# Performance work log

Measured on AMD Instinct MI355X. Metric: run time of the kernel, lower is better.

Reference implementation:

```python
import jax, jax.numpy as jnp
import numpy as np


def _pairwise_sqdist(a, b):
    # a: [m, n, d], b: [m, n, d] -> M: [m, n, n], M[m,i,j] = ||a[m,i]-b[m,j]||^2
    # Use the expansion |a|^2 + |b|^2 - 2 a.b to avoid materializing the
    # [m, n, n, d] difference tensor; clamp tiny negatives from cancellation.
    a2 = jnp.sum(a * a, axis=-1)  # [m, n]
    b2 = jnp.sum(b * b, axis=-1)  # [m, n]
    ab = jnp.einsum('mid,mjd->mij', a, b)  # [m, n, n]
    return jnp.maximum(a2[:, :, None] + b2[:, None, :] - 2.0 * ab, 0.0)


def setup_inputs() -> dict:
    key = jax.random.key(0)
    k1, k2 = jax.random.split(key)
    template = jax.random.normal(k1, (16, 4096, 3), dtype=jnp.float32)
    source = jax.random.normal(k2, (16, 4096, 3), dtype=jnp.float32)
    return {"template": template, "source": source}


def reference(template, source):
    M = _pairwise_sqdist(template, source)  # [m, n, n]
    # min over template index (axis 1): nearest template point for each source point
    dist1 = jnp.mean(jnp.sqrt(jnp.min(M, axis=1)))
    # min over source index (axis 2): nearest source point for each template point
    dist2 = jnp.mean(jnp.sqrt(jnp.min(M, axis=2)))
    return (dist1 + dist2) / 2.0
```

## Files before the change

kernel.cpp:

```cpp
#include <hip/hip_runtime.h>

#define N_PTS   4096
#define N_BATCH 16
#define INV_CNT (1.0f / (2.0f * N_BATCH * N_PTS))
#define AROW_BYTES ((size_t)2 * N_BATCH * N_PTS * 16 * 2)
#define NBLK    1024

typedef _Float16 f16x8  __attribute__((ext_vector_type(8)));

__global__ __launch_bounds__(256) void prep_kernel(
    const float* __restrict__ tpl, const float* __restrict__ src,
    _Float16* __restrict__ arow, float* __restrict__ out) {
    int pt = blockIdx.x * 256 + threadIdx.x;
    if (pt == 0) out[0] = 0.0f;
    const float* p = (pt < 65536 ? tpl : src) + (size_t)(pt & 65535) * 3;
    float x = p[0], y = p[1], z = p[2];
    float o2 = fmaf(x, x, fmaf(y, y, z * z));
    _Float16 xh = (_Float16)x, yh = (_Float16)y, zh = (_Float16)z;
    _Float16 xl = (_Float16)(x - (float)xh);
    _Float16 yl = (_Float16)(y - (float)yh);
    _Float16 zl = (_Float16)(z - (float)zh);
    _Float16 o2h = (_Float16)o2;
    _Float16 o2l = (_Float16)(o2 - (float)o2h);
    const _Float16 m2 = (_Float16)-2.0f;
    f16x8 v0, v1;
    v0[0] = m2 * xh; v0[1] = m2 * yh; v0[2] = m2 * zh;
    v0[3] = m2 * xl; v0[4] = m2 * yl; v0[5] = m2 * zl;
    v0[6] = m2 * xh; v0[7] = m2 * yh;
    v1[0] = m2 * zh; v1[1] = o2h; v1[2] = o2l;
    v1[3] = (_Float16)0.0f; v1[4] = (_Float16)0.0f; v1[5] = (_Float16)0.0f;
    v1[6] = (_Float16)0.0f; v1[7] = (_Float16)0.0f;
    *(f16x8*)(arow + (size_t)pt * 16)     = v0;
    *(f16x8*)(arow + (size_t)pt * 16 + 8) = v1;
}

#define FD(a,x,y) "v_min3_f32 %[" #a "], v" #x ", v" #y ", %[" #a "]\n\t"
#define FOLD_D0 FD(acc0,32,33) FD(acc1,34,35) FD(acc0,36,37) FD(acc1,38,39) \
                FD(acc0,40,41) FD(acc1,42,43) FD(acc0,44,45) FD(acc1,46,47)
#define FOLD_D1 FD(acc0,48,49) FD(acc1,50,51) FD(acc0,52,53) FD(acc1,54,55) \
                FD(acc0,56,57) FD(acc1,58,59) FD(acc0,60,61) FD(acc1,62,63)
#define FOLD_D2 FD(acc0,64,65) FD(acc1,66,67) FD(acc0,68,69) FD(acc1,70,71) \
                FD(acc0,72,73) FD(acc1,74,75) FD(acc0,76,77) FD(acc1,78,79)
#define FOLD_D3 FD(acc0,80,81) FD(acc1,82,83) FD(acc0,84,85) FD(acc1,86,87) \
                FD(acc0,88,89) FD(acc1,90,91) FD(acc0,92,93) FD(acc1,94,95)
#define MF0(a) "v_mfma_f32_32x32x16_f16 v[32:47], %[" #a "], %[bf], v[96:111]\n\t"
#define MF1(a) "v_mfma_f32_32x32x16_f16 v[48:63], %[" #a "], %[bf], v[96:111]\n\t"
#define MF2(a) "v_mfma_f32_32x32x16_f16 v[64:79], %[" #a "], %[bf], v[96:111]\n\t"
#define MF3(a) "v_mfma_f32_32x32x16_f16 v[80:95], %[" #a "], %[bf], v[96:111]\n\t"
#define LD(a,off) "global_load_dwordx4 %[" #a "], %[voff], %[sb] offset:" #off "\n\t"
#define WNOP(n) "s_waitcnt vmcnt(" #n ")\n\t" "s_nop 1\n\t"
#define ZM(r) "v_mov_b32 v" #r ", 0\n\t"

__global__ __launch_bounds__(256, 4) void chamfer_mfma(
    const float* __restrict__ tpl, const float* __restrict__ src,
    const _Float16* __restrict__ arow, float* __restrict__ blocksum,
    float* __restrict__ out) {
    __shared__ float wsum[4];

    const int tid = threadIdx.x;
    const int wv = tid >> 6, lane = tid & 63;
    const int n = lane & 31, g = lane >> 5;
    const int qb = blockIdx.x, batch = blockIdx.y, dir = blockIdx.z;

    const float* qpts = (dir == 0) ? src : tpl;
    const _Float16* abase = arow + ((dir == 0) ? (size_t)0 : (size_t)65536 * 16)
                          + (size_t)batch * 4096 * 16;

    const int q = qb * 128 + wv * 32 + n;
    const float* p = qpts + (size_t)(batch * 4096 + q) * 3;
    float px = p[0], py = p[1], pz = p[2];
    float p2 = fmaf(px, px, fmaf(py, py, pz * pz));
    f16x8 bf;
    {
        _Float16 xh = (_Float16)px, yh = (_Float16)py, zh = (_Float16)pz;
        _Float16 xl = (_Float16)(px - (float)xh);
        _Float16 yl = (_Float16)(py - (float)yh);
        _Float16 zl = (_Float16)(pz - (float)zh);
        if (g == 0) {
            bf[0] = xh; bf[1] = yh; bf[2] = zh;
            bf[3] = xh; bf[4] = yh; bf[5] = zh;
            bf[6] = xl; bf[7] = yl;
        } else {
            bf[0] = zl; bf[1] = (_Float16)1.0f; bf[2] = (_Float16)1.0f;
            bf[3] = (_Float16)0.0f; bf[4] = (_Float16)0.0f; bf[5] = (_Float16)0.0f;
            bf[6] = (_Float16)0.0f; bf[7] = (_Float16)0.0f;
        }
    }

    int voff = n * 32 + g * 16;
    int cnt = 30;
    float acc0 = 1e30f, acc1 = 1e30f;
    f16x8 ra0, ra1, ra2, ra3;

    asm volatile(
        "s_waitcnt vmcnt(0)\n\t"
        ZM(96) ZM(97) ZM(98) ZM(99) ZM(100) ZM(101) ZM(102) ZM(103)
        ZM(104) ZM(105) ZM(106) ZM(107) ZM(108) ZM(109) ZM(110) ZM(111)
        LD(a0,0) LD(a1,1024) LD(a2,2048) LD(a3,3072)
        "v_add_u32 %[voff], 0x1000, %[voff]\n\t"
        "s_waitcnt vmcnt(3)\n\t" MF0(a0) LD(a0,0)
        "s_waitcnt vmcnt(3)\n\t" MF1(a1) LD(a1,1024)
        "s_waitcnt vmcnt(3)\n\t" MF2(a2) LD(a2,2048)
        "s_waitcnt vmcnt(3)\n\t" MF3(a3) LD(a3,3072)
        "L_cham_%=:\n\t"
        "v_add_u32 %[voff], 0x1000, %[voff]\n\t"
        FOLD_D0 WNOP(3) MF0(a0) LD(a0,0)
        FOLD_D1 WNOP(3) MF1(a1) LD(a1,1024)
        FOLD_D2 WNOP(3) MF2(a2) LD(a2,2048)
        FOLD_D3 WNOP(3) MF3(a3) LD(a3,3072)
        "s_sub_u32 %[cnt], %[cnt], 1\n\t"
        "s_cmp_lg_u32 %[cnt], 0\n\t"
        "s_cbranch_scc1 L_cham_%=\n\t"
        FOLD_D0 WNOP(3) MF0(a0)
        FOLD_D1 WNOP(2) MF1(a1)
        FOLD_D2 WNOP(1) MF2(a2)
        FOLD_D3 WNOP(0) MF3(a3)
        FOLD_D0 FOLD_D1 FOLD_D2 FOLD_D3
        : [a0]"=&v"(ra0), [a1]"=&v"(ra1), [a2]"=&v"(ra2), [a3]"=&v"(ra3),
          [voff]"+v"(voff), [cnt]"+s"(cnt), [acc0]"+v"(acc0), [acc1]"+v"(acc1)
        : [bf]"v"(bf), [sb]"s"(abase)
        : "memory", "scc",
          "v32","v33","v34","v35","v36","v37","v38","v39",
          "v40","v41","v42","v43","v44","v45","v46","v47",
          "v48","v49","v50","v51","v52","v53","v54","v55",
          "v56","v57","v58","v59","v60","v61","v62","v63",
          "v64","v65","v66","v67","v68","v69","v70","v71",
          "v72","v73","v74","v75","v76","v77","v78","v79",
          "v80","v81","v82","v83","v84","v85","v86","v87",
          "v88","v89","v90","v91","v92","v93","v94","v95",
          "v96","v97","v98","v99","v100","v101","v102","v103",
          "v104","v105","v106","v107","v108","v109","v110","v111");

    float v = fminf(acc0, acc1);
    v = fminf(v, __shfl_xor(v, 32));
    float d = fmaxf(v + p2, 0.0f);
    float s = sqrtf(d) * INV_CNT;
    if (g != 0) s = 0.0f;
    #pragma unroll
    for (int off = 32; off > 0; off >>= 1) s += __shfl_down(s, off);
    if (lane == 0) wsum[wv] = s;
    __syncthreads();
    if (tid == 0) {
        float t = wsum[0] + wsum[1] + wsum[2] + wsum[3];
        if (blocksum) {
            int flat = (blockIdx.z * N_BATCH + blockIdx.y) * 32 + blockIdx.x;
            blocksum[flat] = t;
        } else {
            atomicAdd(out, t);
        }
    }
}

__global__ __launch_bounds__(256) void final_kernel(
    const float* __restrict__ blocksum, float* __restrict__ out) {
    __shared__ float wsum[4];
    float s = 0.0f;
    #pragma unroll
    for (int j = 0; j < NBLK / 256; ++j)
        s += blocksum[j * 256 + threadIdx.x];
    #pragma unroll
    for (int off = 32; off > 0; off >>= 1) s += __shfl_down(s, off);
    if ((threadIdx.x & 63) == 0) wsum[threadIdx.x >> 6] = s;
    __syncthreads();
    if (threadIdx.x == 0) out[0] = wsum[0] + wsum[1] + wsum[2] + wsum[3];
}

extern "C" void kernel_launch(void* const* d_in, const int* in_sizes, int n_in,
                              void* d_out, int out_size, void* d_ws, size_t ws_size,
                              hipStream_t stream) {
    const float* tpl = (const float*)d_in[0];
    const float* src = (const float*)d_in[1];
    float* out = (float*)d_out;
    _Float16* arow = (_Float16*)d_ws;
    const bool roomy = ws_size >= AROW_BYTES + NBLK * sizeof(float);
    float* blocksum = roomy ? (float*)((char*)d_ws + AROW_BYTES) : nullptr;

    hipLaunchKernelGGL(prep_kernel, dim3((2 * N_BATCH * N_PTS) / 256),
                       dim3(256), 0, stream, tpl, src, arow, out);
    dim3 grid(N_PTS / 128, N_BATCH, 2);
    hipLaunchKernelGGL(chamfer_mfma, grid, dim3(256), 0, stream,
                       tpl, src, arow, blocksum, out);
    if (roomy)
        hipLaunchKernelGGL(final_kernel, dim3(1), dim3(256), 0, stream,
                           blocksum, out);
}
```

Measured before the change: 81.22 us.

## Process two query tiles per wave to reuse loaded A rows across MFMAs

Each wave now handles 64 query points (two B fragments), so every loaded 32-row A tile feeds two MFMAs, halving global loads per MFMA. The pipeline is restructured to eight in-flight loads with interleaved min-folds of the previous tile's accumulators, and the grid is halved, with NBLK and the blocksum indexing updated to match. Occupancy is lowered to 2 waves-per-SIMD bound, and the prefetch overruns the row buffer, so blocksum is moved 8 KB further into the workspace.

```diff
diff --git a/kernel.cpp b/kernel.cpp
--- a/kernel.cpp
+++ b/kernel.cpp
@@ -4,7 +4,7 @@
 #define N_BATCH 16
 #define INV_CNT (1.0f / (2.0f * N_BATCH * N_PTS))
 #define AROW_BYTES ((size_t)2 * N_BATCH * N_PTS * 16 * 2)
-#define NBLK    1024
+#define NBLK    512
 
 typedef _Float16 f16x8  __attribute__((ext_vector_type(8)));
 
@@ -35,23 +35,27 @@
 }
 
 #define FD(a,x,y) "v_min3_f32 %[" #a "], v" #x ", v" #y ", %[" #a "]\n\t"
-#define FOLD_D0 FD(acc0,32,33) FD(acc1,34,35) FD(acc0,36,37) FD(acc1,38,39) \
-                FD(acc0,40,41) FD(acc1,42,43) FD(acc0,44,45) FD(acc1,46,47)
-#define FOLD_D1 FD(acc0,48,49) FD(acc1,50,51) FD(acc0,52,53) FD(acc1,54,55) \
-                FD(acc0,56,57) FD(acc1,58,59) FD(acc0,60,61) FD(acc1,62,63)
-#define FOLD_D2 FD(acc0,64,65) FD(acc1,66,67) FD(acc0,68,69) FD(acc1,70,71) \
-                FD(acc0,72,73) FD(acc1,74,75) FD(acc0,76,77) FD(acc1,78,79)
-#define FOLD_D3 FD(acc0,80,81) FD(acc1,82,83) FD(acc0,84,85) FD(acc1,86,87) \
-                FD(acc0,88,89) FD(acc1,90,91) FD(acc0,92,93) FD(acc1,94,95)
-#define MF0(a) "v_mfma_f32_32x32x16_f16 v[32:47], %[" #a "], %[bf], v[96:111]\n\t"
-#define MF1(a) "v_mfma_f32_32x32x16_f16 v[48:63], %[" #a "], %[bf], v[96:111]\n\t"
-#define MF2(a) "v_mfma_f32_32x32x16_f16 v[64:79], %[" #a "], %[bf], v[96:111]\n\t"
-#define MF3(a) "v_mfma_f32_32x32x16_f16 v[80:95], %[" #a "], %[bf], v[96:111]\n\t"
-#define LD(a,off) "global_load_dwordx4 %[" #a "], %[voff], %[sb] offset:" #off "\n\t"
-#define WNOP(n) "s_waitcnt vmcnt(" #n ")\n\t" "s_nop 1\n\t"
-#define ZM(r) "v_mov_b32 v" #r ", 0\n\t"
+#define FOLD_D0A FD(acc0,32,33) FD(acc1,34,35) FD(acc0,36,37) FD(acc1,38,39) \
+                 FD(acc0,40,41) FD(acc1,42,43) FD(acc0,44,45) FD(acc1,46,47)
+#define FOLD_D0B FD(acc0,48,49) FD(acc1,50,51) FD(acc0,52,53) FD(acc1,54,55) \
+                 FD(acc0,56,57) FD(acc1,58,59) FD(acc0,60,61) FD(acc1,62,63)
+#define FOLD_D1A FD(acc2,64,65) FD(acc3,66,67) FD(acc2,68,69) FD(acc3,70,71) \
+                 FD(acc2,72,73) FD(acc3,74,75) FD(acc2,76,77) FD(acc3,78,79)
+#define FOLD_D1B FD(acc2,80,81) FD(acc3,82,83) FD(acc2,84,85) FD(acc3,86,87) \
+                 FD(acc2,88,89) FD(acc3,90,91) FD(acc2,92,93) FD(acc3,94,95)
+#define LD(s,off) "global_load_dwordx4 %[" #s "], %[voff], %[sb] offset:" #off "\n\t"
+#define TILE_E(s,off) "s_waitcnt vmcnt(7)\n\t" \
+  "v_mfma_f32_32x32x16_f16 v[32:47], %[" #s "], %[bf0], v[96:111]\n\t" \
+  "v_mfma_f32_32x32x16_f16 v[64:79], %[" #s "], %[bf1], v[96:111]\n\t" \
+  LD(s,off) FOLD_D0B FOLD_D1B
+#define TILE_O(s,off) "s_waitcnt vmcnt(7)\n\t" \
+  "v_mfma_f32_32x32x16_f16 v[48:63], %[" #s "], %[bf0], v[96:111]\n\t" \
+  "v_mfma_f32_32x32x16_f16 v[80:95], %[" #s "], %[bf1], v[96:111]\n\t" \
+  LD(s,off) FOLD_D0A FOLD_D1A
+#define ZM(r)  "v_mov_b32 v" #r ", 0\n\t"
+#define IM(r)  "v_mov_b32 v" #r ", 0x7f800000\n\t"
 
-__global__ __launch_bounds__(256, 4) void chamfer_mfma(
+__global__ __launch_bounds__(256, 2) void chamfer_mfma(
     const float* __restrict__ tpl, const float* __restrict__ src,
     const _Float16* __restrict__ arow, float* __restrict__ blocksum,
     float* __restrict__ out) {
@@ -66,59 +70,63 @@
     const _Float16* abase = arow + ((dir == 0) ? (size_t)0 : (size_t)65536 * 16)
                           + (size_t)batch * 4096 * 16;
 
-    const int q = qb * 128 + wv * 32 + n;
-    const float* p = qpts + (size_t)(batch * 4096 + q) * 3;
-    float px = p[0], py = p[1], pz = p[2];
-    float p2 = fmaf(px, px, fmaf(py, py, pz * pz));
-    f16x8 bf;
-    {
+    f16x8 bfr[2];
+    float p2[2];
+    #pragma unroll
+    for (int i = 0; i < 2; ++i) {
+        const int q = qb * 256 + wv * 64 + i * 32 + n;
+        const float* p = qpts + (size_t)(batch * 4096 + q) * 3;
+        float px = p[0], py = p[1], pz = p[2];
+        p2[i] = fmaf(px, px, fmaf(py, py, pz * pz));
         _Float16 xh = (_Float16)px, yh = (_Float16)py, zh = (_Float16)pz;
         _Float16 xl = (_Float16)(px - (float)xh);
         _Float16 yl = (_Float16)(py - (float)yh);
         _Float16 zl = (_Float16)(pz - (float)zh);
+        f16x8 b;
         if (g == 0) {
-            bf[0] = xh; bf[1] = yh; bf[2] = zh;
-            bf[3] = xh; bf[4] = yh; bf[5] = zh;
-            bf[6] = xl; bf[7] = yl;
+            b[0] = xh; b[1] = yh; b[2] = zh;
+            b[3] = xh; b[4] = yh; b[5] = zh;
+            b[6] = xl; b[7] = yl;
         } else {
-            bf[0] = zl; bf[1] = (_Float16)1.0f; bf[2] = (_Float16)1.0f;
-            bf[3] = (_Float16)0.0f; bf[4] = (_Float16)0.0f; bf[5] = (_Float16)0.0f;
-            bf[6] = (_Float16)0.0f; bf[7] = (_Float16)0.0f;
+            b[0] = zl; b[1] = (_Float16)1.0f; b[2] = (_Float16)1.0f;
+            b[3] = (_Float16)0.0f; b[4] = (_Float16)0.0f; b[5] = (_Float16)0.0f;
+            b[6] = (_Float16)0.0f; b[7] = (_Float16)0.0f;
         }
+        bfr[i] = b;
     }
 
     int voff = n * 32 + g * 16;
-    int cnt = 30;
-    float acc0 = 1e30f, acc1 = 1e30f;
-    f16x8 ra0, ra1, ra2, ra3;
+    int cnt = 16;
+    float acc0 = 1e30f, acc1 = 1e30f, acc2 = 1e30f, acc3 = 1e30f;
+    f16x8 r0, r1, r2, r3, r4, r5, r6, r7;
 
     asm volatile(
-        "s_waitcnt vmcnt(0)\n\t"
         ZM(96) ZM(97) ZM(98) ZM(99) ZM(100) ZM(101) ZM(102) ZM(103)
         ZM(104) ZM(105) ZM(106) ZM(107) ZM(108) ZM(109) ZM(110) ZM(111)
-        LD(a0,0) LD(a1,1024) LD(a2,2048) LD(a3,3072)
+        IM(48) IM(49) IM(50) IM(51) IM(52) IM(53) IM(54) IM(55)
+        IM(56) IM(57) IM(58) IM(59) IM(60) IM(61) IM(62) IM(63)
+        IM(80) IM(81) IM(82) IM(83) IM(84) IM(85) IM(86) IM(87)
+        IM(88) IM(89) IM(90) IM(91) IM(92) IM(93) IM(94) IM(95)
+        LD(r0,0) LD(r1,1024) LD(r2,2048) LD(r3,3072)
         "v_add_u32 %[voff], 0x1000, %[voff]\n\t"
-        "s_waitcnt vmcnt(3)\n\t" MF0(a0) LD(a0,0)
-        "s_waitcnt vmcnt(3)\n\t" MF1(a1) LD(a1,1024)
-        "s_waitcnt vmcnt(3)\n\t" MF2(a2) LD(a2,2048)
-        "s_waitcnt vmcnt(3)\n\t" MF3(a3) LD(a3,3072)
+        LD(r4,0) LD(r5,1024) LD(r6,2048) LD(r7,3072)
+        "v_add_u32 %[voff], 0x1000, %[voff]\n\t"
         "L_cham_%=:\n\t"
+        TILE_E(r0,0) TILE_O(r1,1024) TILE_E(r2,2048) TILE_O(r3,3072)
         "v_add_u32 %[voff], 0x1000, %[voff]\n\t"
-        FOLD_D0 WNOP(3) MF0(a0) LD(a0,0)
-        FOLD_D1 WNOP(3) MF1(a1) LD(a1,1024)
-        FOLD_D2 WNOP(3) MF2(a2) LD(a2,2048)
-        FOLD_D3 WNOP(3) MF3(a3) LD(a3,3072)
+        TILE_E(r4,0) TILE_O(r5,1024) TILE_E(r6,2048) TILE_O(r7,3072)
+        "v_add_u32 %[voff], 0x1000, %[voff]\n\t"
         "s_sub_u32 %[cnt], %[cnt], 1\n\t"
         "s_cmp_lg_u32 %[cnt], 0\n\t"
         "s_cbranch_scc1 L_cham_%=\n\t"
-        FOLD_D0 WNOP(3) MF0(a0)
-        FOLD_D1 WNOP(2) MF1(a1)
-        FOLD_D2 WNOP(1) MF2(a2)
-        FOLD_D3 WNOP(0) MF3(a3)
-        FOLD_D0 FOLD_D1 FOLD_D2 FOLD_D3
-        : [a0]"=&v"(ra0), [a1]"=&v"(ra1), [a2]"=&v"(ra2), [a3]"=&v"(ra3),
-          [voff]"+v"(voff), [cnt]"+s"(cnt), [acc0]"+v"(acc0), [acc1]"+v"(acc1)
-        : [bf]"v"(bf), [sb]"s"(abase)
+        "s_nop 7\n\t" "s_nop 7\n\t" "s_nop 7\n\t"
+        FOLD_D0B FOLD_D1B
+        "s_waitcnt vmcnt(0)\n\t"
+        : [r0]"=&v"(r0), [r1]"=&v"(r1), [r2]"=&v"(r2), [r3]"=&v"(r3),
+          [r4]"=&v"(r4), [r5]"=&v"(r5), [r6]"=&v"(r6), [r7]"=&v"(r7),
+          [voff]"+v"(voff), [cnt]"+s"(cnt),
+          [acc0]"+v"(acc0), [acc1]"+v"(acc1), [acc2]"+v"(acc2), [acc3]"+v"(acc3)
+        : [bf0]"v"(bfr[0]), [bf1]"v"(bfr[1]), [sb]"s"(abase)
         : "memory", "scc",
           "v32","v33","v34","v35","v36","v37","v38","v39",
           "v40","v41","v42","v43","v44","v45","v46","v47",
@@ -131,10 +139,13 @@
           "v96","v97","v98","v99","v100","v101","v102","v103",
           "v104","v105","v106","v107","v108","v109","v110","v111");
 
-    float v = fminf(acc0, acc1);
-    v = fminf(v, __shfl_xor(v, 32));
-    float d = fmaxf(v + p2, 0.0f);
-    float s = sqrtf(d) * INV_CNT;
+    float v0 = fminf(acc0, acc1);
+    v0 = fminf(v0, __shfl_xor(v0, 32));
+    float v1 = fminf(acc2, acc3);
+    v1 = fminf(v1, __shfl_xor(v1, 32));
+    float d0 = fmaxf(v0 + p2[0], 0.0f);
+    float d1 = fmaxf(v1 + p2[1], 0.0f);
+    float s = (sqrtf(d0) + sqrtf(d1)) * INV_CNT;
     if (g != 0) s = 0.0f;
     #pragma unroll
     for (int off = 32; off > 0; off >>= 1) s += __shfl_down(s, off);
@@ -143,7 +154,7 @@
     if (tid == 0) {
         float t = wsum[0] + wsum[1] + wsum[2] + wsum[3];
         if (blocksum) {
-            int flat = (blockIdx.z * N_BATCH + blockIdx.y) * 32 + blockIdx.x;
+            int flat = (blockIdx.z * N_BATCH + blockIdx.y) * 16 + blockIdx.x;
             blocksum[flat] = t;
         } else {
             atomicAdd(out, t);
@@ -172,12 +183,12 @@
     const float* src = (const float*)d_in[1];
     float* out = (float*)d_out;
     _Float16* arow = (_Float16*)d_ws;
-    const bool roomy = ws_size >= AROW_BYTES + NBLK * sizeof(float);
-    float* blocksum = roomy ? (float*)((char*)d_ws + AROW_BYTES) : nullptr;
+    const bool roomy = ws_size >= AROW_BYTES + 8192 + NBLK * sizeof(float);
+    float* blocksum = roomy ? (float*)((char*)d_ws + AROW_BYTES + 8192) : nullptr;
 
     hipLaunchKernelGGL(prep_kernel, dim3((2 * N_BATCH * N_PTS) / 256),
                        dim3(256), 0, stream, tpl, src, arow, out);
-    dim3 grid(N_PTS / 128, N_BATCH, 2);
+    dim3 grid(N_PTS / 256, N_BATCH, 2);
     hipLaunchKernelGGL(chamfer_mfma, grid, dim3(256), 0, stream,
                        tpl, src, arow, blocksum, out);
     if (roomy)
```

Measured after the change: 76.80 us. 1.06x faster.
